# Optimization experiments

Hardware: AMD Instinct MI355X
Metric: run time of the kernel (lower is better)

Reference implementation:

```python
import jax, jax.numpy as jnp
import numpy as np

B, LQ, LKV = 2, 2048, 2048
DQ, DKV, HID, NH = 1024, 1024, 1024, 16
HD = HID // NH
EPS = 1e-5


def setup_inputs() -> dict:
    key = jax.random.key(0)
    ks = jax.random.split(key, 12)
    s_q = 1.0 / np.sqrt(DQ)
    s_kv = 1.0 / np.sqrt(DKV)
    s_h = 1.0 / np.sqrt(HID)
    return {
        "query": jax.random.normal(ks[0], (B, LQ, DQ), jnp.float32),
        "key_value": jax.random.normal(ks[1], (B, LKV, DKV), jnp.float32),
        "Wq": jax.random.uniform(ks[2], (DQ, HID), jnp.float32, -s_q, s_q),
        "bq": jax.random.uniform(ks[3], (HID,), jnp.float32, -s_q, s_q),
        "Wk": jax.random.uniform(ks[4], (DKV, HID), jnp.float32, -s_kv, s_kv),
        "bk": jax.random.uniform(ks[5], (HID,), jnp.float32, -s_kv, s_kv),
        "Wv": jax.random.uniform(ks[6], (DKV, HID), jnp.float32, -s_kv, s_kv),
        "bv": jax.random.uniform(ks[7], (HID,), jnp.float32, -s_kv, s_kv),
        "Wo": jax.random.uniform(ks[8], (HID, DQ), jnp.float32, -s_h, s_h),
        "bo": jax.random.uniform(ks[9], (DQ,), jnp.float32, -s_h, s_h),
        "ln_gamma": jnp.ones((DQ,), jnp.float32),
        "ln_beta": jnp.zeros((DQ,), jnp.float32),
    }


def reference(query, key_value, Wq, bq, Wk, bk, Wv, bv, Wo, bo, ln_gamma, ln_beta):
    b, lq, _ = query.shape
    lkv = key_value.shape[1]
    # projections -> [b, heads, len, head_dim]
    Q = (query @ Wq + bq).reshape(b, lq, NH, HD).transpose(0, 2, 1, 3)
    K = (key_value @ Wk + bk).reshape(b, lkv, NH, HD).transpose(0, 2, 1, 3)
    V = (key_value @ Wv + bv).reshape(b, lkv, NH, HD).transpose(0, 2, 1, 3)
    scores = jnp.einsum("bhqd,bhkd->bhqk", Q, K) / jnp.sqrt(jnp.float32(HD))
    attn = jax.nn.softmax(scores, axis=-1)
    ctx = jnp.einsum("bhqk,bhkd->bhqd", attn, V)
    ctx = ctx.transpose(0, 2, 1, 3).reshape(b, lq, HID)
    out = ctx @ Wo + bo
    x = query + out
    mu = jnp.mean(x, axis=-1, keepdims=True)
    var = jnp.mean(jnp.square(x - mu), axis=-1, keepdims=True)
    return (x - mu) / jnp.sqrt(var + EPS) * ln_gamma + ln_beta
```

## Files before the change

kernel.cpp:

```cpp
#include <hip/hip_runtime.h>

typedef unsigned short u16;
typedef __bf16 bf16x8 __attribute__((ext_vector_type(8)));
typedef float f32x4 __attribute__((ext_vector_type(4)));
typedef unsigned short u16x4 __attribute__((ext_vector_type(4)));

#define LOG2E 1.44269504088896340736f
#define LDK 1040
#define LDV 2080
#define EXPM16 12599160.0f

__device__ __forceinline__ u16 f2bf(float f) {
  unsigned u = __float_as_uint(f);
  u += 0x7FFFu + ((u >> 16) & 1u);
  return (u16)(u >> 16);
}

__device__ __forceinline__ void load_lds16(const void* g, void* l) {
  __builtin_amdgcn_global_load_lds(
      (__attribute__((address_space(1))) void*)g,
      (__attribute__((address_space(3))) void*)l, 16, 0, 0);
}

__device__ __forceinline__ f32x4 mfma16(bf16x8 a, bf16x8 b, f32x4 c) {
  return __builtin_amdgcn_mfma_f32_16x16x32_bf16(a, b, c, 0, 0, 0);
}

__global__ __launch_bounds__(256) void pre_kernel(
    const float* __restrict__ q, const float* __restrict__ kv,
    u16* __restrict__ Xq, u16* __restrict__ Xkv,
    const float* __restrict__ Wq, const float* __restrict__ Wk,
    const float* __restrict__ Wv, const float* __restrict__ Wo,
    u16* __restrict__ Wqt, u16* __restrict__ Wkt,
    u16* __restrict__ Wvt, u16* __restrict__ Wot) {
  __shared__ float tile[32][33];
  const int bid = blockIdx.x;
  if (bid < 8192) {
    const int n4each = 4096 * 256;
    int i = bid * 256 + threadIdx.x;
    const float* src; u16* dst; int j;
    if (i < n4each) { src = q; dst = Xq; j = i; }
    else            { src = kv; dst = Xkv; j = i - n4each; }
    const float4 v = ((const float4*)src)[j];
    u16x4 o;
    o.x = f2bf(v.x); o.y = f2bf(v.y); o.z = f2bf(v.z); o.w = f2bf(v.w);
    ((u16x4*)dst)[j] = o;
    return;
  }
  const int t = bid - 8192;
  const int z = t >> 10, rem = t & 1023;
  const float* W; u16* Wt;
  switch (z) {
    case 0: W = Wq; Wt = Wqt; break;
    case 1: W = Wk; Wt = Wkt; break;
    case 2: W = Wv; Wt = Wvt; break;
    default: W = Wo; Wt = Wot; break;
  }
  const int tx = threadIdx.x & 31, ty = threadIdx.x >> 5;
  const int n0 = (rem & 31) * 32, k0 = (rem >> 5) * 32;
#pragma unroll
  for (int i = 0; i < 4; i++)
    tile[ty + i * 8][tx] = W[(size_t)(k0 + ty + i * 8) * 1024 + n0 + tx];
  __syncthreads();
#pragma unroll
  for (int i = 0; i < 4; i++)
    Wt[(size_t)(n0 + ty + i * 8) * 1024 + k0 + tx] = f2bf(tile[tx][ty + i * 8]);
}

__device__ __forceinline__ void gemm_tile(
    const u16* __restrict__ A, int lda, const u16* __restrict__ Bt, int ldb,
    const float* __restrict__ bias, bool brow, float scale,
    u16* __restrict__ Cb, float* __restrict__ Cf,
    int ldc, int bm, int bn, int K) {
  __shared__ alignas(16) u16 As[128 * 32];
  __shared__ alignas(16) u16 Bs[128 * 32];
  const int tid = threadIdx.x;
  const int wave = tid >> 6, lane = tid & 63;
  const int lm = lane & 15, kq = lane >> 4;
  const int g1 = tid, g2 = tid + 256;
  const u16* Ag1 = A + (size_t)(bm + (g1 >> 2)) * lda + (g1 & 3) * 8;
  const u16* Ag2 = A + (size_t)(bm + (g2 >> 2)) * lda + (g2 & 3) * 8;
  const u16* Bg1 = Bt + (size_t)(bn + (g1 >> 2)) * ldb + (g1 & 3) * 8;
  const u16* Bg2 = Bt + (size_t)(bn + (g2 >> 2)) * ldb + (g2 & 3) * 8;
  u16* lA1 = &As[g1 * 8]; u16* lA2 = &As[g2 * 8];
  u16* lB1 = &Bs[g1 * 8]; u16* lB2 = &Bs[g2 * 8];
  const int wm = (wave >> 1) * 64, wn = (wave & 1) * 64;

  f32x4 acc[4][4] = {};
  for (int k0 = 0; k0 < K; k0 += 32) {
    __syncthreads();
    load_lds16(Ag1 + k0, lA1);
    load_lds16(Ag2 + k0, lA2);
    load_lds16(Bg1 + k0, lB1);
    load_lds16(Bg2 + k0, lB2);
    __syncthreads();
    bf16x8 a[4], b[4];
#pragma unroll
    for (int t = 0; t < 4; t++)
      a[t] = *(const bf16x8*)&As[(wm + t * 16 + lm) * 32 + kq * 8];
#pragma unroll
    for (int t = 0; t < 4; t++)
      b[t] = *(const bf16x8*)&Bs[(wn + t * 16 + lm) * 32 + kq * 8];
#pragma unroll
    for (int mt = 0; mt < 4; mt++)
#pragma unroll
      for (int nt = 0; nt < 4; nt++)
        acc[mt][nt] = mfma16(a[mt], b[nt], acc[mt][nt]);
  }
#pragma unroll
  for (int mt = 0; mt < 4; mt++) {
    float rb[4];
#pragma unroll
    for (int r = 0; r < 4; r++)
      rb[r] = (bias && brow) ? bias[bm + wm + mt * 16 + kq * 4 + r] : 0.f;
#pragma unroll
    for (int nt = 0; nt < 4; nt++) {
      const int col = bn + wn + nt * 16 + lm;
      const float cb = (bias && !brow) ? bias[col] : 0.f;
#pragma unroll
      for (int r = 0; r < 4; r++) {
        const int row = bm + wm + mt * 16 + kq * 4 + r;
        const size_t idx = (size_t)row * ldc + col;
        const float v = (acc[mt][nt][r] + rb[r] + cb) * scale;
        if (Cf) Cf[idx] = v;
        else    Cb[idx] = f2bf(v);
      }
    }
  }
}

__global__ __launch_bounds__(256) void proj_gemm_kernel(
    const u16* __restrict__ Xq, const u16* __restrict__ Xkv,
    const u16* __restrict__ Wqt, const u16* __restrict__ Wkt, const u16* __restrict__ Wvt,
    const float* __restrict__ bq, const float* __restrict__ bk, const float* __restrict__ bv,
    u16* __restrict__ Qp, u16* __restrict__ Kp, u16* __restrict__ Vt, float qscale) {
  const int bid = blockIdx.x;
  const u16 *A, *Bt; const float* bias; u16* C;
  bool brow = false; float sc = 1.f; int ldc = 1024; int bm, bn;
  if (bid < 512) {
    const int r = bid & 255;
    const int xcd = r & 7, s = r >> 3;
    bm = (xcd * 4 + (s >> 3)) * 128;
    bn = (s & 7) * 128;
    if (bid < 256) { A = Xq;  Bt = Wqt; bias = bq; C = Qp; sc = qscale; }
    else           { A = Xkv; Bt = Wkt; bias = bk; C = Kp; ldc = LDK;  }
  } else {
    int r = bid - 512;
    const int z = r >> 7; r &= 127;
    const int xcd = r & 7, s = r >> 3;
    bm = (s >> 1) * 128;
    bn = (xcd * 2 + (s & 1)) * 128;
    A = Wvt; Bt = Xkv + (size_t)z * 2048 * 1024; bias = bv; brow = true;
    C = Vt + (size_t)z * 1024 * LDV; ldc = LDV;
  }
  gemm_tile(A, 1024, Bt, 1024, bias, brow, sc, C, nullptr, ldc, bm, bn, 1024);
}

__global__ __launch_bounds__(256) void ogemm_kernel(
    const u16* __restrict__ Ctx, const u16* __restrict__ Wot,
    float* __restrict__ X0, float* __restrict__ X1) {
  const int z = blockIdx.z;
  float* Cf = z ? X1 : X0;
  const int lin = blockIdx.x + 8 * blockIdx.y;
  const int xcd = lin & 7, s = lin >> 3;
  const int bm = (xcd * 4 + (s >> 3)) * 128, bn = (s & 7) * 128;
  gemm_tile(Ctx + z * 512, 1024, Wot + z * 512, 1024, nullptr, false, 1.f,
            nullptr, Cf, 1024, bm, bn, 512);
}

__global__ __launch_bounds__(512, 4) void attn_kernel(
    const u16* __restrict__ Qp, const u16* __restrict__ Kp,
    const u16* __restrict__ Vt, u16* __restrict__ ctx) {
  __shared__ alignas(16) u16 smem[32768];
  const int tid = threadIdx.x;
  const int wave = tid >> 6, lane = tid & 63;
  const int kh = wave >> 2, w4 = wave & 3;
  const int lm = lane & 15, kq = lane >> 4;
  const int L = blockIdx.x;
  const int xcd = L & 7, s = L >> 3;
  const int combo = xcd + 8 * (s >> 4);
  const int qb = s & 15;
  const int h = combo & 15, b = combo >> 4;
  const int qbase = qb * 128 + w4 * 32;

  u16* Ksh = smem + kh * 8192;
  u16* Vsh = smem + 16384 + kh * 8192;

  bf16x8 qf[2][2];
#pragma unroll
  for (int qt = 0; qt < 2; qt++)
#pragma unroll
    for (int kc = 0; kc < 2; kc++)
      qf[qt][kc] = *(const bf16x8*)(Qp + (size_t)(b * 2048 + qbase + qt * 16 + lm) * 1024 +
                                    h * 64 + kc * 32 + kq * 8);

  union { u16 u[8]; bf16x8 v; } uo;
#pragma unroll
  for (int i = 0; i < 8; i++) uo.u[i] = 0x3F80;
  const bf16x8 ones = uo.v;

  const u16* Kb = Kp + ((size_t)b * 2048 + kh * 1024) * LDK + h * 64;
  const u16* Vb = Vt + (size_t)(b * 1024 + h * 64) * LDV + kh * 1024;
  const int sp = lane ^ ((lane >> 3) & 7);
  const int c4 = sp >> 2, c3 = sp & 3;
  const int kvsw = ((lm * 4 + kq) ^ (lm >> 1)) * 8;

  f32x4 o[4][2] = {};
  f32x4 lsum[2] = {};

#pragma unroll
  for (int j = 0; j < 2; j++) {
    const int ii = w4 * 2 + j;
    const u16* gk = Kb + (size_t)(16 * (ii & 3) + c4) * LDK + (ii >> 2) * 32 + c3 * 8;
    load_lds16(gk, &Ksh[ii * 512 + lane * 8]);
    const u16* gv = Vb + (size_t)(16 * (ii & 3) + c4) * LDV + (ii >> 2) * 32 + c3 * 8;
    load_lds16(gv, &Vsh[ii * 512 + lane * 8]);
  }

  int cur = 0;
  for (int t = 0; t < 16; ++t) {
    if (t < 15) {
      const int kvn = (t + 1) * 64;
      const int nb = (cur ^ 1) * 4096;
#pragma unroll
      for (int j = 0; j < 2; j++) {
        const int ii = w4 * 2 + j;
        const u16* gk = Kb + (size_t)(kvn + 16 * (ii & 3) + c4) * LDK + (ii >> 2) * 32 + c3 * 8;
        load_lds16(gk, &Ksh[nb + ii * 512 + lane * 8]);
        const u16* gv = Vb + (size_t)(16 * (ii & 3) + c4) * LDV + kvn + (ii >> 2) * 32 + c3 * 8;
        load_lds16(gv, &Vsh[nb + ii * 512 + lane * 8]);
      }
      __builtin_amdgcn_sched_barrier(0);
      asm volatile("s_waitcnt vmcnt(4)" ::: "memory");
    } else {
      __builtin_amdgcn_sched_barrier(0);
      asm volatile("s_waitcnt vmcnt(0)" ::: "memory");
    }
    __builtin_amdgcn_sched_barrier(0);
    __builtin_amdgcn_s_barrier();

    const int cb = cur * 4096;
    __builtin_amdgcn_s_setprio(1);

    bf16x8 kf[2][4];
#pragma unroll
    for (int kc = 0; kc < 2; kc++)
#pragma unroll
      for (int kvt = 0; kvt < 4; kvt++)
        kf[kc][kvt] = *(const bf16x8*)&Ksh[cb + kc * 2048 + kvt * 512 + kvsw];

    bf16x8 pf[2][2];
#pragma unroll
    for (int qt = 0; qt < 2; qt++) {
      f32x4 st[4] = {};
#pragma unroll
      for (int kc = 0; kc < 2; kc++)
#pragma unroll
        for (int kvt = 0; kvt < 4; kvt++)
          st[kvt] = mfma16(kf[kc][kvt], qf[qt][kc], st[kvt]);
      unsigned Xd[4][2];
#pragma unroll
      for (int kvt = 0; kvt < 4; kvt++) {
        const unsigned e0 = __float_as_uint(fmaf(st[kvt][0], 128.f, EXPM16));
        const unsigned e1 = __float_as_uint(fmaf(st[kvt][1], 128.f, EXPM16));
        const unsigned e2 = __float_as_uint(fmaf(st[kvt][2], 128.f, EXPM16));
        const unsigned e3 = __float_as_uint(fmaf(st[kvt][3], 128.f, EXPM16));
        Xd[kvt][0] = __builtin_amdgcn_perm(e1, e0, 0x05040100u);
        Xd[kvt][1] = __builtin_amdgcn_perm(e3, e2, 0x05040100u);
      }
#pragma unroll
      for (int K1 = 0; K1 < 2; K1++) {
        unsigned a0 = Xd[2 * K1][0], b0 = Xd[2 * K1 + 1][0];
        unsigned a1 = Xd[2 * K1][1], b1 = Xd[2 * K1 + 1][1];
        asm("v_permlane32_swap_b32 %0, %1\n\t"
            "v_permlane16_swap_b32 %0, %1"
            : "+v"(a0), "+v"(b0));
        asm("v_permlane32_swap_b32 %0, %1\n\t"
            "v_permlane16_swap_b32 %0, %1"
            : "+v"(a1), "+v"(b1));
        union { uint4 u; bf16x8 v; } c;
        c.u.x = a0; c.u.y = a1; c.u.z = b0; c.u.w = b1;
        pf[qt][K1] = c.v;
      }
    }
#pragma unroll
    for (int s2 = 0; s2 < 2; s2++) {
      bf16x8 vf[4];
#pragma unroll
      for (int hdt = 0; hdt < 4; hdt++)
        vf[hdt] = *(const bf16x8*)&Vsh[cb + s2 * 2048 + hdt * 512 + kvsw];
#pragma unroll
      for (int qt = 0; qt < 2; qt++) {
        lsum[qt] = mfma16(ones, pf[qt][s2], lsum[qt]);
#pragma unroll
        for (int hdt = 0; hdt < 4; hdt++)
          o[hdt][qt] = mfma16(vf[hdt], pf[qt][s2], o[hdt][qt]);
      }
    }
    __builtin_amdgcn_s_setprio(0);
    __builtin_amdgcn_sched_barrier(0);
    __builtin_amdgcn_s_barrier();
    cur ^= 1;
  }

  __syncthreads();
  float* ex = (float*)smem;
  const int exi = (w4 * 64 + lane) * 36;
  if (kh == 1) {
#pragma unroll
    for (int qt = 0; qt < 2; qt++)
#pragma unroll
      for (int hdt = 0; hdt < 4; hdt++)
        *(f32x4*)&ex[exi + (qt * 4 + hdt) * 4] = o[hdt][qt];
    ex[exi + 32] = lsum[0][0];
    ex[exi + 33] = lsum[1][0];
  }
  __syncthreads();
  if (kh == 0) {
#pragma unroll
    for (int qt = 0; qt < 2; qt++) {
      const float lo = ex[exi + 32 + qt];
      const float rl = 1.f / (lsum[qt][0] + lo);
      u16* cbp = ctx + (size_t)(b * 2048 + qbase + qt * 16 + lm) * 1024 + h * 64 + kq * 4;
#pragma unroll
      for (int hdt = 0; hdt < 4; hdt++) {
        const f32x4 op = *(const f32x4*)&ex[exi + (qt * 4 + hdt) * 4];
        u16x4 w;
#pragma unroll
        for (int r = 0; r < 4; r++) w[r] = f2bf((o[hdt][qt][r] + op[r]) * rl);
        *(u16x4*)(cbp + hdt * 16) = w;
      }
    }
  }
}

__global__ __launch_bounds__(256) void ln_kernel(
    const float* __restrict__ x0, const float* __restrict__ x1,
    const float* __restrict__ q, const float* __restrict__ bo,
    const float* __restrict__ gamma, const float* __restrict__ beta,
    float* __restrict__ out) {
  const int row = blockIdx.x;
  const int t = threadIdx.x;
  const size_t g = (size_t)row * 256 + t;
  const float4 a = ((const float4*)x0)[g];
  const float4 c = ((const float4*)x1)[g];
  const float4 d = ((const float4*)q)[g];
  const float4 bv = ((const float4*)bo)[t];
  float4 v;
  v.x = a.x + c.x + d.x + bv.x;
  v.y = a.y + c.y + d.y + bv.y;
  v.z = a.z + c.z + d.z + bv.z;
  v.w = a.w + c.w + d.w + bv.w;
  float s = v.x + v.y + v.z + v.w;
  float s2 = v.x * v.x + v.y * v.y + v.z * v.z + v.w * v.w;
#pragma unroll
  for (int m = 1; m < 64; m <<= 1) {
    s += __shfl_xor(s, m);
    s2 += __shfl_xor(s2, m);
  }
  __shared__ float red[8];
  const int wave = t >> 6, lane = t & 63;
  if (lane == 0) { red[wave] = s; red[4 + wave] = s2; }
  __syncthreads();
  s = red[0] + red[1] + red[2] + red[3];
  s2 = red[4] + red[5] + red[6] + red[7];
  const float mu = s * (1.f / 1024.f);
  const float var = s2 * (1.f / 1024.f) - mu * mu;
  const float rstd = rsqrtf(var + 1e-5f);
  const float4 gm = ((const float4*)gamma)[t];
  const float4 bt = ((const float4*)beta)[t];
  float4 o;
  o.x = (v.x - mu) * rstd * gm.x + bt.x;
  o.y = (v.y - mu) * rstd * gm.y + bt.y;
  o.z = (v.z - mu) * rstd * gm.z + bt.z;
  o.w = (v.w - mu) * rstd * gm.w + bt.w;
  ((float4*)(out + (size_t)row * 1024))[t] = o;
}

extern "C" void kernel_launch(void* const* d_in, const int* in_sizes, int n_in,
                              void* d_out, int out_size, void* d_ws, size_t ws_size,
                              hipStream_t stream) {
  const float* query     = (const float*)d_in[0];
  const float* key_value = (const float*)d_in[1];
  const float* Wq = (const float*)d_in[2];
  const float* bq = (const float*)d_in[3];
  const float* Wk = (const float*)d_in[4];
  const float* bk = (const float*)d_in[5];
  const float* Wv = (const float*)d_in[6];
  const float* bv = (const float*)d_in[7];
  const float* Wo = (const float*)d_in[8];
  const float* bo = (const float*)d_in[9];
  const float* gamma = (const float*)d_in[10];
  const float* beta  = (const float*)d_in[11];
  float* out = (float*)d_out;

  const size_t MT = (size_t)4096 * 1024;
  const size_t WT = (size_t)1024 * 1024;
  char* ws = (char*)d_ws;
  u16* Xq  = (u16*)ws; ws += MT * 2;
  u16* Xkv = (u16*)ws; ws += MT * 2;
  u16* Wqt = (u16*)ws; ws += WT * 2;
  u16* Wkt = (u16*)ws; ws += WT * 2;
  u16* Wvt = (u16*)ws; ws += WT * 2;
  u16* Wot = (u16*)ws; ws += WT * 2;
  u16* Qp  = (u16*)ws; ws += MT * 2;
  u16* Kp  = (u16*)ws; ws += (size_t)4096 * LDK * 2;
  u16* Vt  = (u16*)ws; ws += (size_t)2048 * LDV * 2;
  float* X0 = (float*)ws; ws += MT * 4;
  float* X1 = (float*)ws; ws += MT * 4;
  u16* Ctx = Xq;

  const float qscale = 0.125f * LOG2E;

  pre_kernel<<<12288, 256, 0, stream>>>(query, key_value, Xq, Xkv,
                                        Wq, Wk, Wv, Wo, Wqt, Wkt, Wvt, Wot);
  proj_gemm_kernel<<<768, 256, 0, stream>>>(Xq, Xkv, Wqt, Wkt, Wvt, bq, bk, bv,
                                            Qp, Kp, Vt, qscale);
  attn_kernel<<<512, 512, 0, stream>>>(Qp, Kp, Vt, Ctx);
  ogemm_kernel<<<dim3(8, 32, 2), 256, 0, stream>>>(Ctx, Wot, X0, X1);
  ln_kernel<<<4096, 256, 0, stream>>>(X0, X1, query, bo, gamma, beta, out);
}
```

Measured before the change: 215.5 us.

## Double-buffer GEMM LDS tiles to overlap global loads with MFMA

The projection GEMM tile now uses two LDS buffers for A and B and issues the next K-slice's global-to-LDS loads before computing the current one. Partial vmcnt waits and raw s_barrier calls replace the two __syncthreads per iteration, so load latency can hide behind the MFMA work. It also raises wave priority during the MFMA block. In exchange LDS use doubles, which may lower occupancy, and correctness depends on the hand-written waitcnt values matching the number of loads in flight.

New measurement: 213.5 us. About the same (-1.0%).

```diff
diff --git a/kernel.cpp b/kernel.cpp
--- a/kernel.cpp
+++ b/kernel.cpp
@@ -72,8 +72,8 @@
     const float* __restrict__ bias, bool brow, float scale,
     u16* __restrict__ Cb, float* __restrict__ Cf,
     int ldc, int bm, int bn, int K) {
-  __shared__ alignas(16) u16 As[128 * 32];
-  __shared__ alignas(16) u16 Bs[128 * 32];
+  __shared__ alignas(16) u16 As[2][128 * 32];
+  __shared__ alignas(16) u16 Bs[2][128 * 32];
   const int tid = threadIdx.x;
   const int wave = tid >> 6, lane = tid & 63;
   const int lm = lane & 15, kq = lane >> 4;
@@ -82,30 +82,48 @@
   const u16* Ag2 = A + (size_t)(bm + (g2 >> 2)) * lda + (g2 & 3) * 8;
   const u16* Bg1 = Bt + (size_t)(bn + (g1 >> 2)) * ldb + (g1 & 3) * 8;
   const u16* Bg2 = Bt + (size_t)(bn + (g2 >> 2)) * ldb + (g2 & 3) * 8;
-  u16* lA1 = &As[g1 * 8]; u16* lA2 = &As[g2 * 8];
-  u16* lB1 = &Bs[g1 * 8]; u16* lB2 = &Bs[g2 * 8];
   const int wm = (wave >> 1) * 64, wn = (wave & 1) * 64;
 
+  load_lds16(Ag1, &As[0][g1 * 8]);
+  load_lds16(Ag2, &As[0][g2 * 8]);
+  load_lds16(Bg1, &Bs[0][g1 * 8]);
+  load_lds16(Bg2, &Bs[0][g2 * 8]);
+
   f32x4 acc[4][4] = {};
+  int cur = 0;
   for (int k0 = 0; k0 < K; k0 += 32) {
-    __syncthreads();
-    load_lds16(Ag1 + k0, lA1);
-    load_lds16(Ag2 + k0, lA2);
-    load_lds16(Bg1 + k0, lB1);
-    load_lds16(Bg2 + k0, lB2);
-    __syncthreads();
+    if (k0 + 32 < K) {
+      const int nxt = cur ^ 1;
+      load_lds16(Ag1 + k0 + 32, &As[nxt][g1 * 8]);
+      load_lds16(Ag2 + k0 + 32, &As[nxt][g2 * 8]);
+      load_lds16(Bg1 + k0 + 32, &Bs[nxt][g1 * 8]);
+      load_lds16(Bg2 + k0 + 32, &Bs[nxt][g2 * 8]);
+      __builtin_amdgcn_sched_barrier(0);
+      asm volatile("s_waitcnt vmcnt(4)" ::: "memory");
+    } else {
+      __builtin_amdgcn_sched_barrier(0);
+      asm volatile("s_waitcnt vmcnt(0)" ::: "memory");
+    }
+    __builtin_amdgcn_sched_barrier(0);
+    __builtin_amdgcn_s_barrier();
+
+    __builtin_amdgcn_s_setprio(1);
     bf16x8 a[4], b[4];
 #pragma unroll
     for (int t = 0; t < 4; t++)
-      a[t] = *(const bf16x8*)&As[(wm + t * 16 + lm) * 32 + kq * 8];
+      a[t] = *(const bf16x8*)&As[cur][(wm + t * 16 + lm) * 32 + kq * 8];
 #pragma unroll
     for (int t = 0; t < 4; t++)
-      b[t] = *(const bf16x8*)&Bs[(wn + t * 16 + lm) * 32 + kq * 8];
+      b[t] = *(const bf16x8*)&Bs[cur][(wn + t * 16 + lm) * 32 + kq * 8];
 #pragma unroll
     for (int mt = 0; mt < 4; mt++)
 #pragma unroll
       for (int nt = 0; nt < 4; nt++)
         acc[mt][nt] = mfma16(a[mt], b[nt], acc[mt][nt]);
+    __builtin_amdgcn_s_setprio(0);
+    __builtin_amdgcn_sched_barrier(0);
+    __builtin_amdgcn_s_barrier();
+    cur ^= 1;
   }
 #pragma unroll
   for (int mt = 0; mt < 4; mt++) {
```

## Replace split-K output GEMM with full-K 64x128 tiles and drop partial buffer

Applied to the files above, without the earlier changes.

The output projection GEMM previously split K into two halves, writing two fp32 partial results that the LayerNorm kernel summed. It is now a dedicated kernel using 64x128 tiles over the full K=1024, launched as 512 blocks and writing a single fp32 buffer, so LayerNorm reads one fewer 16 MB tensor. This removes the extra partial-sum write and read traffic. In exchange the new kernel uses a simple single-buffered LDS loop with two barriers per k-step and scalar stores, which may hurt GEMM efficiency.

After: 208.7 us. 3.2% less time.

```diff
diff --git a/kernel.cpp b/kernel.cpp
--- a/kernel.cpp
+++ b/kernel.cpp
@@ -158,14 +158,55 @@
 
 __global__ __launch_bounds__(256) void ogemm_kernel(
     const u16* __restrict__ Ctx, const u16* __restrict__ Wot,
-    float* __restrict__ X0, float* __restrict__ X1) {
-  const int z = blockIdx.z;
-  float* Cf = z ? X1 : X0;
-  const int lin = blockIdx.x + 8 * blockIdx.y;
+    float* __restrict__ X) {
+  __shared__ alignas(16) u16 As[64 * 32];
+  __shared__ alignas(16) u16 Bs[128 * 32];
+  const int tid = threadIdx.x;
+  const int wave = tid >> 6, lane = tid & 63;
+  const int lm = lane & 15, kq = lane >> 4;
+  const int lin = blockIdx.x;
   const int xcd = lin & 7, s = lin >> 3;
-  const int bm = (xcd * 4 + (s >> 3)) * 128, bn = (s & 7) * 128;
-  gemm_tile(Ctx + z * 512, 1024, Wot + z * 512, 1024, nullptr, false, 1.f,
-            nullptr, Cf, 1024, bm, bn, 512);
+  const int bm = (xcd * 8 + (s >> 3)) * 64;
+  const int bn = (s & 7) * 128;
+  const int g1 = tid, g2 = tid + 256;
+  const u16* Ag  = Ctx + (size_t)(bm + (g1 >> 2)) * 1024 + (g1 & 3) * 8;
+  const u16* Bg1 = Wot + (size_t)(bn + (g1 >> 2)) * 1024 + (g1 & 3) * 8;
+  const u16* Bg2 = Wot + (size_t)(bn + (g2 >> 2)) * 1024 + (g2 & 3) * 8;
+  u16* lA  = &As[g1 * 8];
+  u16* lB1 = &Bs[g1 * 8]; u16* lB2 = &Bs[g2 * 8];
+  const int wm = (wave >> 1) * 32, wn = (wave & 1) * 64;
+
+  f32x4 acc[2][4] = {};
+  for (int k0 = 0; k0 < 1024; k0 += 32) {
+    __syncthreads();
+    load_lds16(Ag + k0, lA);
+    load_lds16(Bg1 + k0, lB1);
+    load_lds16(Bg2 + k0, lB2);
+    __syncthreads();
+    bf16x8 a[2], b[4];
+#pragma unroll
+    for (int t = 0; t < 2; t++)
+      a[t] = *(const bf16x8*)&As[(wm + t * 16 + lm) * 32 + kq * 8];
+#pragma unroll
+    for (int t = 0; t < 4; t++)
+      b[t] = *(const bf16x8*)&Bs[(wn + t * 16 + lm) * 32 + kq * 8];
+#pragma unroll
+    for (int mt = 0; mt < 2; mt++)
+#pragma unroll
+      for (int nt = 0; nt < 4; nt++)
+        acc[mt][nt] = mfma16(a[mt], b[nt], acc[mt][nt]);
+  }
+#pragma unroll
+  for (int mt = 0; mt < 2; mt++)
+#pragma unroll
+    for (int nt = 0; nt < 4; nt++) {
+      const int col = bn + wn + nt * 16 + lm;
+#pragma unroll
+      for (int r = 0; r < 4; r++) {
+        const int row = bm + wm + mt * 16 + kq * 4 + r;
+        X[(size_t)row * 1024 + col] = acc[mt][nt][r];
+      }
+    }
 }
 
 __global__ __launch_bounds__(512, 4) void attn_kernel(
@@ -335,7 +376,7 @@
 }
 
 __global__ __launch_bounds__(256) void ln_kernel(
-    const float* __restrict__ x0, const float* __restrict__ x1,
+    const float* __restrict__ x0,
     const float* __restrict__ q, const float* __restrict__ bo,
     const float* __restrict__ gamma, const float* __restrict__ beta,
     float* __restrict__ out) {
@@ -343,14 +384,13 @@
   const int t = threadIdx.x;
   const size_t g = (size_t)row * 256 + t;
   const float4 a = ((const float4*)x0)[g];
-  const float4 c = ((const float4*)x1)[g];
   const float4 d = ((const float4*)q)[g];
   const float4 bv = ((const float4*)bo)[t];
   float4 v;
-  v.x = a.x + c.x + d.x + bv.x;
-  v.y = a.y + c.y + d.y + bv.y;
-  v.z = a.z + c.z + d.z + bv.z;
-  v.w = a.w + c.w + d.w + bv.w;
+  v.x = a.x + d.x + bv.x;
+  v.y = a.y + d.y + bv.y;
+  v.z = a.z + d.z + bv.z;
+  v.w = a.w + d.w + bv.w;
   float s = v.x + v.y + v.z + v.w;
   float s2 = v.x * v.x + v.y * v.y + v.z * v.z + v.w * v.w;
 #pragma unroll
@@ -407,7 +447,6 @@
   u16* Kp  = (u16*)ws; ws += (size_t)4096 * LDK * 2;
   u16* Vt  = (u16*)ws; ws += (size_t)2048 * LDV * 2;
   float* X0 = (float*)ws; ws += MT * 4;
-  float* X1 = (float*)ws; ws += MT * 4;
   u16* Ctx = Xq;
 
   const float qscale = 0.125f * LOG2E;
@@ -417,6 +456,6 @@
   proj_gemm_kernel<<<768, 256, 0, stream>>>(Xq, Xkv, Wqt, Wkt, Wvt, bq, bk, bv,
                                             Qp, Kp, Vt, qscale);
   attn_kernel<<<512, 512, 0, stream>>>(Qp, Kp, Vt, Ctx);
-  ogemm_kernel<<<dim3(8, 32, 2), 256, 0, stream>>>(Ctx, Wot, X0, X1);
-  ln_kernel<<<4096, 256, 0, stream>>>(X0, X1, query, bo, gamma, beta, out);
-}
+  ogemm_kernel<<<512, 256, 0, stream>>>(Ctx, Wot, X0);
+  ln_kernel<<<4096, 256, 0, stream>>>(X0, query, bo, gamma, beta, out);
+}
```
